# Performance work log

Hardware: AMD Instinct MI355X
Metric: run time of the kernel (lower is better)

Reference implementation:

```python
import math
import jax, jax.numpy as jnp
import numpy as np

IN_CH = 64
NUM_ANCHOR = 4
MAP_H, MAP_W = 96, 96
BATCH = 8
BN_EPS = 1e-5


def _conv2d(x, w, b, padding, dilation):
    # x: [B,C,H,W], w: [O,I,kh,kw] (OIHW)
    y = jax.lax.conv_general_dilated(
        x, w, window_strides=(1, 1),
        padding=((padding, padding), (padding, padding)),
        rhs_dilation=(dilation, dilation),
        dimension_numbers=('NCHW', 'OIHW', 'NCHW'))
    return y + b[None, :, None, None]


def _bn(x, gamma, beta, mean, var):
    scale = gamma / jnp.sqrt(var + BN_EPS)
    return x * scale[None, :, None, None] + (beta - mean * scale)[None, :, None, None]


def setup_inputs() -> dict:
    key = jax.random.key(0)
    ks = jax.random.split(key, 12)
    # cyclic channel-shift permutation matrices, one per anchor pass
    eye = np.eye(IN_CH, dtype=np.float32)
    shift = IN_CH // (2 * NUM_ANCHOR)
    perms = np.stack([eye[np.roll(np.arange(IN_CH), i * shift)] for i in range(2 * NUM_ANCHOR)])
    w_std = 1.0 / math.sqrt(IN_CH * 9)
    return {
        'x': jax.random.normal(ks[0], (BATCH, IN_CH, MAP_H, MAP_W), dtype=jnp.float32),
        'perms': jnp.asarray(perms),
        'dcn_w': jax.random.normal(ks[1], (IN_CH, IN_CH, 3, 3), dtype=jnp.float32) * w_std,
        'dcn_b': jax.random.normal(ks[2], (IN_CH,), dtype=jnp.float32) * 0.01,
        'conv2_w': jax.random.normal(ks[3], (IN_CH, IN_CH, 3, 3), dtype=jnp.float32) * w_std,
        'conv2_b': jax.random.normal(ks[4], (IN_CH,), dtype=jnp.float32) * 0.01,
        'conv3_w': jax.random.normal(ks[5], (IN_CH, IN_CH, 3, 3), dtype=jnp.float32) * w_std,
        'conv3_b': jax.random.normal(ks[6], (IN_CH,), dtype=jnp.float32) * 0.01,
        'bn_gamma': jax.random.uniform(ks[7], (3, IN_CH), dtype=jnp.float32, minval=0.5, maxval=1.5),
        'bn_beta': jax.random.normal(ks[8], (3, IN_CH), dtype=jnp.float32) * 0.1,
        'bn_mean': jax.random.normal(ks[9], (3, IN_CH), dtype=jnp.float32) * 0.1,
        'bn_var': jax.random.uniform(ks[10], (3, IN_CH), dtype=jnp.float32, minval=0.5, maxval=1.5),
    }


def reference(x, perms, dcn_w, dcn_b, conv2_w, conv2_b, conv3_w, conv3_b,
              bn_gamma, bn_beta, bn_mean, bn_var):
    h = x.shape[2]
    pad = math.ceil(h / (2 ** 1.5 + 2))  # 20 for h=96

    def conv_stack(o):
        # DCN at init (zero offsets) == plain 3x3 conv, pad=1
        o = jax.nn.relu(_bn(_conv2d(o, dcn_w, dcn_b, 1, 1), bn_gamma[0], bn_beta[0], bn_mean[0], bn_var[0]))
        o = jax.nn.relu(_bn(_conv2d(o, conv2_w, conv2_b, 2, 2), bn_gamma[1], bn_beta[1], bn_mean[1], bn_var[1]))
        o = jax.nn.relu(_bn(_conv2d(o, conv3_w, conv3_b, 2, 2), bn_gamma[2], bn_beta[2], bn_mean[2], bn_var[2]))
        return o

    outs = []
    for i in range(2 * NUM_ANCHOR):  # fixed small structural loop
        o = jnp.einsum('mn,bnhw->bmhw', perms[i], x)  # channel permutation
        if i % 2 != 0:
            o = jnp.pad(o, ((0, 0), (0, 0), (pad, pad), (pad, pad)))
        o = jnp.rot90(o, k=i % 4, axes=(-2, -1))   # ccw rotate
        o = conv_stack(o)
        o = jnp.rot90(o, k=(-i) % 4, axes=(-2, -1))  # cw rotate back
        if i % 2 != 0:
            H, W = o.shape[-2], o.shape[-1]
            sh, sw = (H - MAP_H) // 2, (W - MAP_W) // 2
            o = o[..., sh:sh + MAP_H, sw:sw + MAP_W]  # center crop
        outs.append(o)
    out_tensor = jnp.concatenate(outs, axis=1)  # [B, 8*C, H, W]
    out = jnp.max(out_tensor, axis=1, keepdims=True)
    # branch_name == 'midpoint', orientational_anchor=False -> clamped sigmoid
    return jnp.clip(jax.nn.sigmoid(out), 1e-4, 1.0 - 1e-4)
```

## Files before the change

kernel.cpp:

```cpp
#include <hip/hip_runtime.h>
#include <math.h>

#define B 8
#define C 64
#define HW 96
#define NWV 36864

typedef __attribute__((ext_vector_type(8)))  short short8;
typedef __attribute__((ext_vector_type(16))) float floatx16;

__device__ __forceinline__ unsigned short f2bf(float f) {
    unsigned int u = __float_as_uint(f);
    unsigned int r = (u + 0x7fffu + ((u >> 16) & 1u)) >> 16;
    return (unsigned short)r;
}

__device__ __forceinline__ void rotmap(int k, int ta, int tb, int& sa, int& sb) {
    switch (k) {
        case 0: sa = ta;     sb = tb;     break;
        case 1: sa = 2 - tb; sb = ta;     break;
        case 2: sa = 2 - ta; sb = 2 - tb; break;
        default: sa = tb;    sb = 2 - ta; break;
    }
}


__global__ void prep_w(const float* __restrict__ dcn_w, const float* __restrict__ c2w,
                       const float* __restrict__ c3w,
                       const float* __restrict__ gamma, const float* __restrict__ var_,
                       unsigned short* __restrict__ Wall) {
    int idx = blockIdx.x * 256 + threadIdx.x;
    if (idx >= 16 * NWV) return;
    int v = idx / NWV, rem = idx % NWV;
    int tap  = rem >> 12;
    int w12  = rem & 4095;
    int ks   = w12 >> 10;
    int cf   = (w12 >> 9) & 1;
    int lane = (w12 >> 3) & 63;
    int j    = w12 & 7;
    int co = cf * 32 + (lane & 31);
    int ci = ks * 16 + (lane >> 5) * 8 + j;
    int ta = tap / 3, tb = tap % 3;
    const float* src; int k, srcci, l;
    if (v < 8)       { k = v & 3;  srcci = (ci + 8 * v) & 63; src = dcn_w; l = 0; }
    else if (v < 12) { k = v - 8;  srcci = ci; src = c2w; l = 1; }
    else             { k = v - 12; srcci = ci; src = c3w; l = 2; }
    int sa, sb; rotmap(k, ta, tb, sa, sb);
    float s = gamma[l * 64 + co] * rsqrtf(var_[l * 64 + co] + 1e-5f);
    Wall[idx] = f2bf(src[((co * 64 + srcci) * 3 + sa) * 3 + sb] * s);
}

__global__ void prep_bias(const float* __restrict__ dcn_b, const float* __restrict__ c2b,
                          const float* __restrict__ c3b,
                          const float* __restrict__ gamma, const float* __restrict__ beta,
                          const float* __restrict__ mean, const float* __restrict__ var_,
                          float* __restrict__ biasg) {
    int t = threadIdx.x;
    if (t < 192) {
        int l = t >> 6, c = t & 63;
        const float* cb = (l == 0) ? dcn_b : ((l == 1) ? c2b : c3b);
        float s = gamma[l * 64 + c] * rsqrtf(var_[l * 64 + c] + 1e-5f);
        biasg[t] = cb[c] * s + beta[l * 64 + c] - mean[l * 64 + c] * s;
    }
}

__global__ __launch_bounds__(256) void prep_x(const float* __restrict__ in,
                                              unsigned short* __restrict__ out) {
    __shared__ float row[64 * 97];
    int by = blockIdx.x;
    int b = by / 96, y = by % 96;
    int t = threadIdx.x;
    for (int e = t; e < 6144; e += 256) {
        int c = e / 96, x = e - c * 96;
        row[c * 97 + x] = in[(((size_t)(b * 64 + c) * 96 + y) * 96) + x];
    }
    __syncthreads();
    for (int e = t; e < 6144; e += 256) {
        int x = e >> 6, c = e & 63;
        out[(((size_t)(b * 96 + y) * 96 + x) << 6) + c] = f2bf(row[c * 97 + x]);
    }
}

template<int LAYER>
__global__ __launch_bounds__(256, 2) void conv_t(
    const unsigned short* __restrict__ in, unsigned short* __restrict__ outb,
    float* __restrict__ maxb,
    const unsigned short* __restrict__ Wall, const float* __restrict__ biasg) {

    constexpr int DIL = (LAYER == 0) ? 1 : 2;
    constexpr int WT  = 32 + 2 * DIL;
    constexpr int RT  = 16 + 2 * DIL;
    constexpr int NR  = 4 + 2 * DIL;

    __shared__ __align__(16) unsigned short xt[RT * WT * 32];
    __shared__ float bs[64];

    int z  = blockIdx.z;
    int br = z >> 3;
    int b  = z & 7;
    int odd = br & 1;

    int Hin, Hout, shift;
    if (LAYER == 0)      { Hin = 96;             Hout = odd ? 104 : 96; shift = odd ? -4 : 0; }
    else if (LAYER == 1) { Hin = odd ? 104 : 96; Hout = odd ? 100 : 96; shift = odd ?  2 : 0; }
    else                 { Hin = odd ? 100 : 96; Hout = 96;             shift = odd ?  2 : 0; }

    int oy0 = blockIdx.y * 16;
    int ox0 = blockIdx.x * 32;
    if (oy0 >= Hout || ox0 >= Hout) return;

    int variant = (LAYER == 0) ? br : ((LAYER == 1) ? 8 + (br & 3) : 12 + (br & 3));
    const short8* Ag = (const short8*)(Wall + (size_t)variant * NWV);

    size_t in_stride = (LAYER == 0) ? (size_t)96 * 96 * 64
                     : (LAYER == 1) ? (size_t)104 * 104 * 64
                                    : (size_t)100 * 100 * 64;
    const unsigned short* inb = in + ((LAYER == 0) ? (size_t)b : (size_t)z) * in_stride;

    int t = threadIdx.x;
    if (t < 64) bs[t] = biasg[LAYER * 64 + t];

    int lane = t & 63, wv = t >> 6;
    int n  = lane & 31;
    int kq = lane >> 5;
    int rowbase = wv << 2;

    floatx16 acc[2][4];
#pragma unroll
    for (int cf = 0; cf < 2; cf++)
#pragma unroll
        for (int pf = 0; pf < 4; pf++)
#pragma unroll
            for (int i = 0; i < 16; i++) acc[cf][pf][i] = 0.f;

    for (int s = 0; s < 2; s++) {
        if (s) __syncthreads();
        for (int e = t; e < RT * WT * 4; e += 256) {
            int p = e >> 2, g = e & 3;
            int yy = p / WT, xx = p - yy * WT;
            int gy = oy0 + shift - DIL + yy;
            int gx = ox0 + shift - DIL + xx;
            uint4 v = make_uint4(0u, 0u, 0u, 0u);
            if ((unsigned)gy < (unsigned)Hin && (unsigned)gx < (unsigned)Hin)
                v = *(const uint4*)(inb + (((size_t)(gy * Hin + gx)) << 6) + (s << 5) + (g << 3));
            *(uint4*)(&xt[(p << 5) + ((g ^ (xx & 3)) << 3)]) = v;
        }
        __syncthreads();

#pragma unroll
        for (int tb = 0; tb < 3; tb++) {
#pragma unroll
            for (int kl = 0; kl < 2; kl++) {
                int ksg = s * 2 + kl;
                short8 a[3][2];
#pragma unroll
                for (int ta = 0; ta < 3; ta++)
#pragma unroll
                    for (int cf = 0; cf < 2; cf++)
                        a[ta][cf] = Ag[(((ta * 3 + tb) * 4 + ksg) * 2 + cf) * 64 + lane];

                int xb = n + tb * DIL;
                int cidx = ((kl * 2 + kq) ^ (xb & 3)) << 3;
                short8 bf[NR];
#pragma unroll
                for (int rr = 0; rr < NR; rr++)
                    bf[rr] = *(const short8*)(&xt[((((rowbase + rr) * WT + xb)) << 5) + cidx]);
#pragma unroll
                for (int ta = 0; ta < 3; ta++)
#pragma unroll
                    for (int pf = 0; pf < 4; pf++) {
                        int rr = pf + ta * DIL;
                        acc[0][pf] = __builtin_amdgcn_mfma_f32_32x32x16_bf16(a[ta][0], bf[rr], acc[0][pf], 0, 0, 0);
                        acc[1][pf] = __builtin_amdgcn_mfma_f32_32x32x16_bf16(a[ta][1], bf[rr], acc[1][pf], 0, 0, 0);
                    }
            }
        }
    }

    if (LAYER < 2) {
        unsigned short* ob = outb + (size_t)z * ((LAYER == 0) ? (size_t)104 * 104 * 64
                                                              : (size_t)100 * 100 * 64);
        int ox = ox0 + n;
#pragma unroll
        for (int pf = 0; pf < 4; pf++) {
            int oy = oy0 + rowbase + pf;
            if (oy < Hout && ox < Hout) {
                size_t pbase = ((size_t)(oy * Hout + ox)) << 6;
#pragma unroll
                for (int cf = 0; cf < 2; cf++)
#pragma unroll
                    for (int rb = 0; rb < 4; rb++) {
                        int co0 = cf * 32 + 4 * kq + 8 * rb;
                        float v0 = fmaxf(acc[cf][pf][rb * 4 + 0] + bs[co0 + 0], 0.f);
                        float v1 = fmaxf(acc[cf][pf][rb * 4 + 1] + bs[co0 + 1], 0.f);
                        float v2 = fmaxf(acc[cf][pf][rb * 4 + 2] + bs[co0 + 2], 0.f);
                        float v3 = fmaxf(acc[cf][pf][rb * 4 + 3] + bs[co0 + 3], 0.f);
                        unsigned int lo = (unsigned int)f2bf(v0) | ((unsigned int)f2bf(v1) << 16);
                        unsigned int hi = (unsigned int)f2bf(v2) | ((unsigned int)f2bf(v3) << 16);
                        *(uint2*)(ob + pbase + co0) = make_uint2(lo, hi);
                    }
            }
        }
    } else {
#pragma unroll
        for (int pf = 0; pf < 4; pf++) {
            float mx = 0.f;
#pragma unroll
            for (int cf = 0; cf < 2; cf++)
#pragma unroll
                for (int rb = 0; rb < 4; rb++)
#pragma unroll
                    for (int i = 0; i < 4; i++) {
                        int co = cf * 32 + 4 * kq + 8 * rb + i;
                        mx = fmaxf(mx, acc[cf][pf][rb * 4 + i] + bs[co]);
                    }
            mx = fmaxf(mx, __shfl_xor(mx, 32, 64));
            if (lane < 32) {
                int oy = oy0 + rowbase + pf;
                maxb[((size_t)z * 96 + oy) * 96 + ox0 + n] = mx;
            }
        }
    }
}

__global__ void final_k(const float* __restrict__ maxb, float* __restrict__ out) {
    int i = blockIdx.x * 256 + threadIdx.x;
    if (i < B * HW * HW) {
        int b = i / 9216, yx = i - b * 9216;
        float m = 0.f;
#pragma unroll
        for (int br = 0; br < 8; br++)
            m = fmaxf(m, maxb[((size_t)(br * 8 + b)) * 9216 + yx]);
        float v = 1.f / (1.f + expf(-m));
        out[i] = fminf(fmaxf(v, 1e-4f), 1.f - 1e-4f);
    }
}


extern "C" void kernel_launch(void* const* d_in, const int* in_sizes, int n_in,
                              void* d_out, int out_size, void* d_ws, size_t ws_size,
                              hipStream_t stream) {
    const float* x     = (const float*)d_in[0];
    const float* dcn_w = (const float*)d_in[2];
    const float* dcn_b = (const float*)d_in[3];
    const float* c2w   = (const float*)d_in[4];
    const float* c2b   = (const float*)d_in[5];
    const float* c3w   = (const float*)d_in[6];
    const float* c3b   = (const float*)d_in[7];
    const float* gamma = (const float*)d_in[8];
    const float* beta  = (const float*)d_in[9];
    const float* mean  = (const float*)d_in[10];
    const float* var_  = (const float*)d_in[11];

    char* ws = (char*)d_ws;
    unsigned short* Wall = (unsigned short*)ws;
    size_t off = (size_t)16 * NWV * 2;
    float* biasg = (float*)(ws + off);            off += 1024;
    float* maxb  = (float*)(ws + off);            off += (size_t)64 * 9216 * 4;
    unsigned short* xhwc = (unsigned short*)(ws + off); off += (size_t)B * 9216 * 64 * 2;
    unsigned short* buf1 = (unsigned short*)(ws + off); off += (size_t)64 * 104 * 104 * 64 * 2;
    unsigned short* buf2 = (unsigned short*)(ws + off);

    prep_w<<<(16 * NWV + 255) / 256, 256, 0, stream>>>(dcn_w, c2w, c3w, gamma, var_, Wall);
    prep_bias<<<1, 256, 0, stream>>>(dcn_b, c2b, c3b, gamma, beta, mean, var_, biasg);
    prep_x<<<B * 96, 256, 0, stream>>>(x, xhwc);

    dim3 g01(4, 7, 64);
    conv_t<0><<<g01, 256, 0, stream>>>(xhwc, buf1, nullptr, Wall, biasg);
    conv_t<1><<<g01, 256, 0, stream>>>(buf1, buf2, nullptr, Wall, biasg);
    dim3 g2(3, 6, 64);
    conv_t<2><<<g2, 256, 0, stream>>>(buf2, nullptr, maxb, Wall, biasg);

    final_k<<<(B * HW * HW + 255) / 256, 256, 0, stream>>>(maxb, (float*)d_out);
}
```

Baseline: 351.8 us.

## Fuse conv2 and conv3 into one kernel with shared-memory intermediate

Replaces the templated per-layer conv kernel with a dedicated conv1 kernel and a fused conv2+conv3 kernel. The fused kernel computes the conv2 output tile plus its halo into LDS and feeds conv3 from there, so the second intermediate buffer never goes to global memory. Conv1 now writes a unified 104x104 padded buffer for all branches, with a separate border-clear kernel and LDS-staged coalesced stores, and software-prefetches the second channel half in registers. The cost is recomputing conv2 on halo pixels, heavy LDS use and higher register pressure at 512 threads per block.

```diff
diff --git a/kernel.cpp b/kernel.cpp
--- a/kernel.cpp
+++ b/kernel.cpp
@@ -23,7 +23,6 @@
         default: sa = tb;    sb = 2 - ta; break;
     }
 }
-
 
 __global__ void prep_w(const float* __restrict__ dcn_w, const float* __restrict__ c2w,
                        const float* __restrict__ c3w,
@@ -81,145 +80,319 @@
     }
 }
 
-template<int LAYER>
-__global__ __launch_bounds__(256, 2) void conv_t(
-    const unsigned short* __restrict__ in, unsigned short* __restrict__ outb,
-    float* __restrict__ maxb,
+__global__ __launch_bounds__(256) void border_clear(unsigned short* __restrict__ buf1) {
+    int idx = blockIdx.y;
+    int br = (idx >> 3) * 2, b = idx & 7;
+    int z = br * 8 + b;
+    int i = blockIdx.x * 32 + (threadIdx.x >> 3);
+    int g = threadIdx.x & 7;
+    int r, c;
+    if (i < 416)      { r = i / 104;              c = i % 104; }
+    else if (i < 832) { int j = i - 416; r = 100 + j / 104; c = j % 104; }
+    else              { int j = i - 832; r = 4 + (j >> 3); int c8 = j & 7;
+                        c = (c8 < 4) ? c8 : 92 + c8; }
+    uint4 zero = make_uint4(0u, 0u, 0u, 0u);
+    *(uint4*)(buf1 + (size_t)z * (104 * 104 * 64) + ((size_t)(r * 104 + c) << 6) + (g << 3)) = zero;
+}
+
+__global__ __launch_bounds__(256, 2) void conv1_k(
+    const unsigned short* __restrict__ xhwc, unsigned short* __restrict__ buf1,
     const unsigned short* __restrict__ Wall, const float* __restrict__ biasg) {
 
-    constexpr int DIL = (LAYER == 0) ? 1 : 2;
-    constexpr int WT  = 32 + 2 * DIL;
-    constexpr int RT  = 16 + 2 * DIL;
-    constexpr int NR  = 4 + 2 * DIL;
-
-    __shared__ __align__(16) unsigned short xt[RT * WT * 32];
-    __shared__ float bs[64];
-
-    int z  = blockIdx.z;
-    int br = z >> 3;
-    int b  = z & 7;
-    int odd = br & 1;
-
-    int Hin, Hout, shift;
-    if (LAYER == 0)      { Hin = 96;             Hout = odd ? 104 : 96; shift = odd ? -4 : 0; }
-    else if (LAYER == 1) { Hin = odd ? 104 : 96; Hout = odd ? 100 : 96; shift = odd ?  2 : 0; }
-    else                 { Hin = odd ? 100 : 96; Hout = 96;             shift = odd ?  2 : 0; }
-
-    int oy0 = blockIdx.y * 16;
-    int ox0 = blockIdx.x * 32;
-    if (oy0 >= Hout || ox0 >= Hout) return;
-
-    int variant = (LAYER == 0) ? br : ((LAYER == 1) ? 8 + (br & 3) : 12 + (br & 3));
-    const short8* Ag = (const short8*)(Wall + (size_t)variant * NWV);
-
-    size_t in_stride = (LAYER == 0) ? (size_t)96 * 96 * 64
-                     : (LAYER == 1) ? (size_t)104 * 104 * 64
-                                    : (size_t)100 * 100 * 64;
-    const unsigned short* inb = in + ((LAYER == 0) ? (size_t)b : (size_t)z) * in_stride;
-
-    int t = threadIdx.x;
-    if (t < 64) bs[t] = biasg[LAYER * 64 + t];
-
-    int lane = t & 63, wv = t >> 6;
-    int n  = lane & 31;
-    int kq = lane >> 5;
-    int rowbase = wv << 2;
-
-    floatx16 acc[2][4];
+    __shared__ __align__(16) unsigned short xt[10 * 34 * 64];
+
+    int z = blockIdx.z, br = z >> 3, b = z & 7, odd = br & 1;
+    int fy0 = blockIdx.y * 8, fx0 = blockIdx.x * 32;
+    int t = threadIdx.x, lane = t & 63, wv = t >> 6;
+    int n = lane & 31, kq = lane >> 5;
+
+    const unsigned short* xb = xhwc + ((size_t)b * 96 * 96 << 6);
+    const short8* Ag = (const short8*)(Wall + (size_t)br * NWV);
+
+    for (int e = t; e < 2720; e += 256) {
+        int p = e >> 3, g = e & 7;
+        int yy = p / 34, xx = p - yy * 34;
+        int gy = fy0 - 5 + yy, gx = fx0 - 5 + xx;
+        uint4 v = make_uint4(0u, 0u, 0u, 0u);
+        if ((unsigned)gy < 96u && (unsigned)gx < 96u)
+            v = *(const uint4*)(xb + ((size_t)(gy * 96 + gx) << 6) + (g << 3));
+        *(uint4*)(xt + (p << 6) + ((g ^ (xx & 7)) << 3)) = v;
+    }
+    __syncthreads();
+
+    floatx16 acc[2][2];
 #pragma unroll
     for (int cf = 0; cf < 2; cf++)
 #pragma unroll
-        for (int pf = 0; pf < 4; pf++)
+        for (int pf = 0; pf < 2; pf++)
 #pragma unroll
             for (int i = 0; i < 16; i++) acc[cf][pf][i] = 0.f;
 
+#pragma unroll
+    for (int ks = 0; ks < 4; ks++) {
+#pragma unroll
+        for (int tb = 0; tb < 3; tb++) {
+            short8 a[3][2];
+#pragma unroll
+            for (int ta = 0; ta < 3; ta++)
+#pragma unroll
+                for (int cf = 0; cf < 2; cf++)
+                    a[ta][cf] = Ag[(((ta * 3 + tb) * 4 + ks) * 2 + cf) * 64 + lane];
+            int xx = n + tb;
+            int g = ((ks * 2 + kq) ^ (xx & 7)) << 3;
+            short8 bf[4];
+#pragma unroll
+            for (int rr = 0; rr < 4; rr++) {
+                int p = (2 * wv + rr) * 34 + xx;
+                bf[rr] = *(const short8*)(xt + (p << 6) + g);
+            }
+#pragma unroll
+            for (int ta = 0; ta < 3; ta++)
+#pragma unroll
+                for (int pf = 0; pf < 2; pf++) {
+                    int rr = pf + ta;
+                    acc[0][pf] = __builtin_amdgcn_mfma_f32_32x32x16_bf16(a[ta][0], bf[rr], acc[0][pf], 0, 0, 0);
+                    acc[1][pf] = __builtin_amdgcn_mfma_f32_32x32x16_bf16(a[ta][1], bf[rr], acc[1][pf], 0, 0, 0);
+                }
+        }
+    }
+
+    float4 bv[2][4];
+#pragma unroll
+    for (int cf = 0; cf < 2; cf++)
+#pragma unroll
+        for (int rb = 0; rb < 4; rb++)
+            bv[cf][rb] = *(const float4*)(biasg + 32 * cf + 8 * rb + 4 * kq);
+
+    __syncthreads();
+#pragma unroll
+    for (int pf = 0; pf < 2; pf++) {
+        int pq = (2 * wv + pf) * 32 + n;
+        int key = (pq & 7) << 1;
+#pragma unroll
+        for (int cf = 0; cf < 2; cf++)
+#pragma unroll
+            for (int rb = 0; rb < 4; rb++) {
+                int u = kq + 2 * rb + 8 * cf;
+                float v0 = fmaxf(acc[cf][pf][rb * 4 + 0] + bv[cf][rb].x, 0.f);
+                float v1 = fmaxf(acc[cf][pf][rb * 4 + 1] + bv[cf][rb].y, 0.f);
+                float v2 = fmaxf(acc[cf][pf][rb * 4 + 2] + bv[cf][rb].z, 0.f);
+                float v3 = fmaxf(acc[cf][pf][rb * 4 + 3] + bv[cf][rb].w, 0.f);
+                uint2 pk = make_uint2((unsigned)f2bf(v0) | ((unsigned)f2bf(v1) << 16),
+                                      (unsigned)f2bf(v2) | ((unsigned)f2bf(v3) << 16));
+                *(uint2*)((char*)xt + pq * 128 + ((u ^ key) << 3)) = pk;
+            }
+    }
+    __syncthreads();
+
+    unsigned short* fb = buf1 + (size_t)z * (104 * 104 * 64);
+    int lo = odd ? 0 : 4, hi = odd ? 104 : 100;
+    for (int e = t; e < 2048; e += 256) {
+        int px = e >> 3, g = e & 7;
+        int key = (px & 7) << 1;
+        uint4 v = *(const uint4*)((const char*)xt + px * 128 + (((2 * g) ^ key) << 3));
+        int lr = px >> 5, nn = px & 31;
+        int f = fy0 + lr, fc = fx0 + nn;
+        if (f >= lo && f < hi && fc >= lo && fc < hi)
+            *(uint4*)(fb + ((size_t)(f * 104 + fc) << 6) + (g << 3)) = v;
+    }
+}
+
+__global__ __launch_bounds__(512, 2) void conv23_k(
+    const unsigned short* __restrict__ buf1, float* __restrict__ maxb,
+    const unsigned short* __restrict__ Wall, const float* __restrict__ biasg) {
+
+    __shared__ __align__(16) unsigned short c2out[768 * 64];
+    __shared__ __align__(16) unsigned short xs[960 * 32];
+
+    int z = blockIdx.z, br = z >> 3, odd = br & 1;
+    int oy0 = blockIdx.y * 16, ox0 = blockIdx.x * 32;
+    int t = threadIdx.x, lane = t & 63, wv = t >> 6;
+    int n = lane & 31, kq = lane >> 5;
+
+    const unsigned short* fb = buf1 + (size_t)z * (104 * 104 * 64);
+    const short8* A2 = (const short8*)(Wall + (size_t)(8  + (br & 3)) * NWV);
+    const short8* A3 = (const short8*)(Wall + (size_t)(12 + (br & 3)) * NWV);
+
+    for (int e = t; e < 3840; e += 512) {
+        int p = e >> 2, g = e & 3;
+        int yy = p / 40, xx = p - yy * 40;
+        uint4 v = *(const uint4*)(fb + ((size_t)((oy0 + yy) * 104 + ox0 + xx) << 6) + (g << 3));
+        *(uint4*)(xs + (p << 5) + ((g ^ (xx & 3)) << 3)) = v;
+    }
+    __syncthreads();
+
+    uint4 pfv[8];
+#pragma unroll
+    for (int k = 0; k < 8; k++) {
+        int e = t + k * 512;
+        if (e < 3840) {
+            int p = e >> 2, g = e & 3;
+            int yy = p / 40, xx = p - yy * 40;
+            pfv[k] = *(const uint4*)(fb + ((size_t)((oy0 + yy) * 104 + ox0 + xx) << 6) + 32 + (g << 3));
+        }
+    }
+
+    int q_[3], row2_[3], col2_[3];
+#pragma unroll
+    for (int jj = 0; jj < 3; jj++) {
+        int q = 96 * wv + 32 * jj + n;
+        q_[jj] = q;
+        int qc = (q < 720) ? q : 719;
+        int r2 = qc / 36;
+        row2_[jj] = r2;
+        col2_[jj] = qc - 36 * r2;
+    }
+
+    floatx16 acc2[3][2];
+#pragma unroll
+    for (int jj = 0; jj < 3; jj++)
+#pragma unroll
+        for (int cf = 0; cf < 2; cf++)
+#pragma unroll
+            for (int i = 0; i < 16; i++) acc2[jj][cf][i] = 0.f;
+
+#pragma unroll
     for (int s = 0; s < 2; s++) {
-        if (s) __syncthreads();
-        for (int e = t; e < RT * WT * 4; e += 256) {
-            int p = e >> 2, g = e & 3;
-            int yy = p / WT, xx = p - yy * WT;
-            int gy = oy0 + shift - DIL + yy;
-            int gx = ox0 + shift - DIL + xx;
-            uint4 v = make_uint4(0u, 0u, 0u, 0u);
-            if ((unsigned)gy < (unsigned)Hin && (unsigned)gx < (unsigned)Hin)
-                v = *(const uint4*)(inb + (((size_t)(gy * Hin + gx)) << 6) + (s << 5) + (g << 3));
-            *(uint4*)(&xt[(p << 5) + ((g ^ (xx & 3)) << 3)]) = v;
-        }
-        __syncthreads();
-
+        if (s == 1) {
+            __syncthreads();
+#pragma unroll
+            for (int k = 0; k < 8; k++) {
+                int e = t + k * 512;
+                if (e < 3840) {
+                    int p = e >> 2, g = e & 3;
+                    int xx2 = p - (p / 40) * 40;
+                    *(uint4*)(xs + (p << 5) + ((g ^ (xx2 & 3)) << 3)) = pfv[k];
+                }
+            }
+            __syncthreads();
+        }
+#pragma unroll
+        for (int kl = 0; kl < 2; kl++) {
+            int ks = s * 2 + kl;
+#pragma unroll
+            for (int tb = 0; tb < 3; tb++) {
+                short8 a[3][2];
+#pragma unroll
+                for (int ta = 0; ta < 3; ta++)
+#pragma unroll
+                    for (int cf = 0; cf < 2; cf++)
+                        a[ta][cf] = A2[(((ta * 3 + tb) * 4 + ks) * 2 + cf) * 64 + lane];
+#pragma unroll
+                for (int jj = 0; jj < 3; jj++) {
+                    int colx = col2_[jj] + 2 * tb;
+                    int gsw = ((kl * 2 + kq) ^ (colx & 3)) << 3;
+#pragma unroll
+                    for (int ta = 0; ta < 3; ta++) {
+                        int p = (row2_[jj] + 2 * ta) * 40 + colx;
+                        short8 bfr = *(const short8*)(xs + (p << 5) + gsw);
+                        acc2[jj][0] = __builtin_amdgcn_mfma_f32_32x32x16_bf16(a[ta][0], bfr, acc2[jj][0], 0, 0, 0);
+                        acc2[jj][1] = __builtin_amdgcn_mfma_f32_32x32x16_bf16(a[ta][1], bfr, acc2[jj][1], 0, 0, 0);
+                    }
+                }
+            }
+        }
+    }
+
+    int rlo2 = (!odd && oy0 == 0)  ? 2  : 0;
+    int rhi2 = (!odd && oy0 == 80) ? 18 : 20;
+    int clo2 = (!odd && ox0 == 0)  ? 2  : 0;
+    int chi2 = (!odd && ox0 == 64) ? 34 : 36;
+    float4 bv2[2][4];
+#pragma unroll
+    for (int cf = 0; cf < 2; cf++)
+#pragma unroll
+        for (int rb = 0; rb < 4; rb++)
+            bv2[cf][rb] = *(const float4*)(biasg + 64 + 32 * cf + 8 * rb + 4 * kq);
+
+#pragma unroll
+    for (int jj = 0; jj < 3; jj++) {
+        if (q_[jj] < 720) {
+            bool valid = (row2_[jj] >= rlo2) && (row2_[jj] < rhi2) &&
+                         (col2_[jj] >= clo2) && (col2_[jj] < chi2);
+            int key = col2_[jj] & 14;
+#pragma unroll
+            for (int cf = 0; cf < 2; cf++)
+#pragma unroll
+                for (int rb = 0; rb < 4; rb++) {
+                    int u = kq + 2 * rb + 8 * cf;
+                    float v0 = 0.f, v1 = 0.f, v2 = 0.f, v3 = 0.f;
+                    if (valid) {
+                        v0 = fmaxf(acc2[jj][cf][rb * 4 + 0] + bv2[cf][rb].x, 0.f);
+                        v1 = fmaxf(acc2[jj][cf][rb * 4 + 1] + bv2[cf][rb].y, 0.f);
+                        v2 = fmaxf(acc2[jj][cf][rb * 4 + 2] + bv2[cf][rb].z, 0.f);
+                        v3 = fmaxf(acc2[jj][cf][rb * 4 + 3] + bv2[cf][rb].w, 0.f);
+                    }
+                    uint2 pk = make_uint2((unsigned)f2bf(v0) | ((unsigned)f2bf(v1) << 16),
+                                          (unsigned)f2bf(v2) | ((unsigned)f2bf(v3) << 16));
+                    *(uint2*)((char*)c2out + q_[jj] * 128 + ((u ^ key) << 3)) = pk;
+                }
+        }
+    }
+    __syncthreads();
+
+    int r0 = 2 * wv;
+    floatx16 acc3[2][2];
+#pragma unroll
+    for (int cf = 0; cf < 2; cf++)
+#pragma unroll
+        for (int pf = 0; pf < 2; pf++)
+#pragma unroll
+            for (int i = 0; i < 16; i++) acc3[cf][pf][i] = 0.f;
+
+#pragma unroll
+    for (int ks = 0; ks < 4; ks++) {
 #pragma unroll
         for (int tb = 0; tb < 3; tb++) {
-#pragma unroll
-            for (int kl = 0; kl < 2; kl++) {
-                int ksg = s * 2 + kl;
-                short8 a[3][2];
-#pragma unroll
-                for (int ta = 0; ta < 3; ta++)
-#pragma unroll
-                    for (int cf = 0; cf < 2; cf++)
-                        a[ta][cf] = Ag[(((ta * 3 + tb) * 4 + ksg) * 2 + cf) * 64 + lane];
-
-                int xb = n + tb * DIL;
-                int cidx = ((kl * 2 + kq) ^ (xb & 3)) << 3;
-                short8 bf[NR];
-#pragma unroll
-                for (int rr = 0; rr < NR; rr++)
-                    bf[rr] = *(const short8*)(&xt[((((rowbase + rr) * WT + xb)) << 5) + cidx]);
-#pragma unroll
-                for (int ta = 0; ta < 3; ta++)
-#pragma unroll
-                    for (int pf = 0; pf < 4; pf++) {
-                        int rr = pf + ta * DIL;
-                        acc[0][pf] = __builtin_amdgcn_mfma_f32_32x32x16_bf16(a[ta][0], bf[rr], acc[0][pf], 0, 0, 0);
-                        acc[1][pf] = __builtin_amdgcn_mfma_f32_32x32x16_bf16(a[ta][1], bf[rr], acc[1][pf], 0, 0, 0);
-                    }
-            }
-        }
-    }
-
-    if (LAYER < 2) {
-        unsigned short* ob = outb + (size_t)z * ((LAYER == 0) ? (size_t)104 * 104 * 64
-                                                              : (size_t)100 * 100 * 64);
-        int ox = ox0 + n;
-#pragma unroll
-        for (int pf = 0; pf < 4; pf++) {
-            int oy = oy0 + rowbase + pf;
-            if (oy < Hout && ox < Hout) {
-                size_t pbase = ((size_t)(oy * Hout + ox)) << 6;
+            short8 a[3][2];
+#pragma unroll
+            for (int ta = 0; ta < 3; ta++)
 #pragma unroll
                 for (int cf = 0; cf < 2; cf++)
-#pragma unroll
-                    for (int rb = 0; rb < 4; rb++) {
-                        int co0 = cf * 32 + 4 * kq + 8 * rb;
-                        float v0 = fmaxf(acc[cf][pf][rb * 4 + 0] + bs[co0 + 0], 0.f);
-                        float v1 = fmaxf(acc[cf][pf][rb * 4 + 1] + bs[co0 + 1], 0.f);
-                        float v2 = fmaxf(acc[cf][pf][rb * 4 + 2] + bs[co0 + 2], 0.f);
-                        float v3 = fmaxf(acc[cf][pf][rb * 4 + 3] + bs[co0 + 3], 0.f);
-                        unsigned int lo = (unsigned int)f2bf(v0) | ((unsigned int)f2bf(v1) << 16);
-                        unsigned int hi = (unsigned int)f2bf(v2) | ((unsigned int)f2bf(v3) << 16);
-                        *(uint2*)(ob + pbase + co0) = make_uint2(lo, hi);
-                    }
-            }
-        }
-    } else {
-#pragma unroll
-        for (int pf = 0; pf < 4; pf++) {
-            float mx = 0.f;
-#pragma unroll
-            for (int cf = 0; cf < 2; cf++)
-#pragma unroll
-                for (int rb = 0; rb < 4; rb++)
-#pragma unroll
-                    for (int i = 0; i < 4; i++) {
-                        int co = cf * 32 + 4 * kq + 8 * rb + i;
-                        mx = fmaxf(mx, acc[cf][pf][rb * 4 + i] + bs[co]);
-                    }
-            mx = fmaxf(mx, __shfl_xor(mx, 32, 64));
-            if (lane < 32) {
-                int oy = oy0 + rowbase + pf;
-                maxb[((size_t)z * 96 + oy) * 96 + ox0 + n] = mx;
-            }
-        }
+                    a[ta][cf] = A3[(((ta * 3 + tb) * 4 + ks) * 2 + cf) * 64 + lane];
+            int col = n + 2 * tb;
+            int key = col & 14;
+            int ublk = 2 * (ks * 2 + kq);
+            short8 bf[6];
+#pragma unroll
+            for (int rr = 0; rr < 6; rr++) {
+                int q = (r0 + rr) * 36 + col;
+                bf[rr] = *(const short8*)((const char*)c2out + q * 128 + ((ublk ^ key) << 3));
+            }
+#pragma unroll
+            for (int ta = 0; ta < 3; ta++)
+#pragma unroll
+                for (int pf = 0; pf < 2; pf++) {
+                    int rr = pf + 2 * ta;
+                    acc3[0][pf] = __builtin_amdgcn_mfma_f32_32x32x16_bf16(a[ta][0], bf[rr], acc3[0][pf], 0, 0, 0);
+                    acc3[1][pf] = __builtin_amdgcn_mfma_f32_32x32x16_bf16(a[ta][1], bf[rr], acc3[1][pf], 0, 0, 0);
+                }
+        }
+    }
+
+    float4 bv3[2][4];
+#pragma unroll
+    for (int cf = 0; cf < 2; cf++)
+#pragma unroll
+        for (int rb = 0; rb < 4; rb++)
+            bv3[cf][rb] = *(const float4*)(biasg + 128 + 32 * cf + 8 * rb + 4 * kq);
+
+#pragma unroll
+    for (int pf = 0; pf < 2; pf++) {
+        float m = 0.f;
+#pragma unroll
+        for (int cf = 0; cf < 2; cf++)
+#pragma unroll
+            for (int rb = 0; rb < 4; rb++) {
+                m = fmaxf(m, acc3[cf][pf][rb * 4 + 0] + bv3[cf][rb].x);
+                m = fmaxf(m, acc3[cf][pf][rb * 4 + 1] + bv3[cf][rb].y);
+                m = fmaxf(m, acc3[cf][pf][rb * 4 + 2] + bv3[cf][rb].z);
+                m = fmaxf(m, acc3[cf][pf][rb * 4 + 3] + bv3[cf][rb].w);
+            }
+        m = fmaxf(m, 0.f);
+        m = fmaxf(m, __shfl_xor(m, 32, 64));
+        if (lane < 32)
+            maxb[((size_t)z * 96 + oy0 + r0 + pf) * 96 + ox0 + n] = m;
     }
 }
 
@@ -258,18 +431,18 @@
     float* biasg = (float*)(ws + off);            off += 1024;
     float* maxb  = (float*)(ws + off);            off += (size_t)64 * 9216 * 4;
     unsigned short* xhwc = (unsigned short*)(ws + off); off += (size_t)B * 9216 * 64 * 2;
-    unsigned short* buf1 = (unsigned short*)(ws + off); off += (size_t)64 * 104 * 104 * 64 * 2;
-    unsigned short* buf2 = (unsigned short*)(ws + off);
+    unsigned short* buf1 = (unsigned short*)(ws + off);
 
     prep_w<<<(16 * NWV + 255) / 256, 256, 0, stream>>>(dcn_w, c2w, c3w, gamma, var_, Wall);
     prep_bias<<<1, 256, 0, stream>>>(dcn_b, c2b, c3b, gamma, beta, mean, var_, biasg);
     prep_x<<<B * 96, 256, 0, stream>>>(x, xhwc);
-
-    dim3 g01(4, 7, 64);
-    conv_t<0><<<g01, 256, 0, stream>>>(xhwc, buf1, nullptr, Wall, biasg);
-    conv_t<1><<<g01, 256, 0, stream>>>(buf1, buf2, nullptr, Wall, biasg);
-    dim3 g2(3, 6, 64);
-    conv_t<2><<<g2, 256, 0, stream>>>(buf2, nullptr, maxb, Wall, biasg);
+    border_clear<<<dim3(50, 32), 256, 0, stream>>>(buf1);
+
+    dim3 g1(4, 13, 64);
+    conv1_k<<<g1, 256, 0, stream>>>(xhwc, buf1, Wall, biasg);
+
+    dim3 g23(3, 6, 64);
+    conv23_k<<<g23, 512, 0, stream>>>(buf1, maxb, Wall, biasg);
 
     final_k<<<(B * HW * HW + 255) / 256, 256, 0, stream>>>(maxb, (float*)d_out);
 }
```

Result: faster. 310.5 us (-11.7%).
